# Kernel optimization log

Measured on AMD Instinct MI355X. Metric: run time of the kernel, lower is better.

The kernel has to match this reference:

```python
import jax, jax.numpy as jnp
import numpy as np

N_HEAD = 16
N_KV_HEAD = 4
HEAD_DIM = 128
D_MODEL = 2048
ROTARY_DIM = 128  # == head_dim
ROTARY_BASE = 10000
N_CTX = 2048
BATCH = 2
SEQ = 2048


def _rope_sincos(T, dtype):
    # Matches calculate_sin_cos_rotary with rotary_adjacent_pairs=False:
    # freq = base**(d/(rd/2)) for d in [0, rd/2), then tiled twice.
    pos = jnp.arange(T, dtype=jnp.float32)
    dim = jnp.arange(ROTARY_DIM // 2, dtype=jnp.float32)
    freq = jnp.asarray(ROTARY_BASE, jnp.float32) ** (dim / (ROTARY_DIM / 2))
    freq = jnp.concatenate([freq, freq])          # [rd]
    angles = pos[:, None] / freq[None, :]          # [T, rd]
    return jnp.sin(angles).astype(dtype), jnp.cos(angles).astype(dtype)


def _rotate_half(x):
    # rotate_every_two with adjacent_pairs=False: [-x2, x1] over halves
    n = x.shape[-1] // 2
    return jnp.concatenate([-x[..., n:], x[..., :n]], axis=-1)


def setup_inputs() -> dict:
    key = jax.random.key(0)
    kx, kq, kkv, kp = jax.random.split(key, 4)
    scale = 0.02
    return {
        "x": jax.random.normal(kx, (BATCH, SEQ, D_MODEL), jnp.float32),
        "Wq": jax.random.normal(kq, (D_MODEL, D_MODEL), jnp.float32) * scale,
        "Wkv": jax.random.normal(kkv, (2 * N_KV_HEAD * HEAD_DIM, D_MODEL), jnp.float32) * scale,
        "Wproj": jax.random.normal(kp, (D_MODEL, D_MODEL), jnp.float32) * scale,
    }


def reference(x, Wq, Wkv, Wproj):
    B, T, C = x.shape
    # QKV projections (torch Linear: y = x @ W.T)
    q = x @ Wq.T                                   # [B,T,C]
    kv = x @ Wkv.T                                 # [B,T,2*kv*hd]
    k, v = jnp.split(kv, 2, axis=2)
    q = q.reshape(B, T, N_HEAD, HEAD_DIM).transpose(0, 2, 1, 3)      # [B,H,T,d]
    k = k.reshape(B, T, N_KV_HEAD, HEAD_DIM).transpose(0, 2, 1, 3)   # [B,Hk,T,d]
    v = v.reshape(B, T, N_KV_HEAD, HEAD_DIM).transpose(0, 2, 1, 3)

    # RoPE: position_ids = arange(T) clamped at n_ctx-1 (identity for T<=n_ctx)
    sin, cos = _rope_sincos(T, q.dtype)            # [T, rd]
    sin = sin[None, None]                          # [1,1,T,rd]
    cos = cos[None, None]
    q = q * cos + _rotate_half(q) * sin
    k = k * cos + _rotate_half(k) * sin

    # GQA: expand kv heads (repeat_interleave along head dim)
    rep = N_HEAD // N_KV_HEAD
    k = jnp.repeat(k, rep, axis=1)                 # [B,H,T,d]
    v = jnp.repeat(v, rep, axis=1)

    # Causal SDPA
    scale = 1.0 / np.sqrt(HEAD_DIM)
    scores = jnp.einsum('bhqd,bhkd->bhqk', q, k) * scale
    causal = jnp.tril(jnp.ones((T, T), bool))
    scores = jnp.where(causal[None, None], scores, jnp.asarray(-jnp.inf, scores.dtype))
    attn = jax.nn.softmax(scores, axis=-1)
    y = jnp.einsum('bhqk,bhkd->bhqd', attn, v)     # [B,H,T,d]

    y = y.transpose(0, 2, 1, 3).reshape(B, T, C)
    return y @ Wproj.T
```

## Files before the change

kernel.cpp:

```cpp
#include <hip/hip_runtime.h>
#include <stdint.h>

#define T_SEQ 2048
#define D_MODEL 2048
#define N_KV 4
#define HD 128
#define QKV_W 3072

typedef unsigned short us;
typedef __attribute__((ext_vector_type(8))) short bf16x8;
typedef __attribute__((ext_vector_type(4))) float f32x4;
typedef __attribute__((ext_vector_type(8))) unsigned short u16x8;

__device__ __forceinline__ us f2bf(float f) {
  union { float f; unsigned int u; } v; v.f = f;
  unsigned int r = v.u + 0x7FFFu + ((v.u >> 16) & 1u);
  return (us)(r >> 16);
}
__device__ __forceinline__ float bf2f(us h) {
  union { unsigned int u; float f; } v; v.u = ((unsigned int)h) << 16;
  return v.f;
}

__device__ __forceinline__ void load_lds16(const void* g, void* l) {
  __builtin_amdgcn_global_load_lds(
      (const __attribute__((address_space(1))) void*)g,
      (__attribute__((address_space(3))) void*)l, 16, 0, 0);
}

__global__ void fill_diag(float* __restrict__ out, float val, int n) {
  int i = blockIdx.x * blockDim.x + threadIdx.x;
  if (i < n) out[i] = val;
}

__global__ void cast_f32_bf16(const float* __restrict__ src,
                              us* __restrict__ dst, int n8) {
  int i = blockIdx.x * blockDim.x + threadIdx.x;
  if (i >= n8) return;
  const float4* s = (const float4*)src + (size_t)i * 2;
  float4 a = s[0], b = s[1];
  u16x8 o;
  o[0] = f2bf(a.x); o[1] = f2bf(a.y); o[2] = f2bf(a.z); o[3] = f2bf(a.w);
  o[4] = f2bf(b.x); o[5] = f2bf(b.y); o[6] = f2bf(b.z); o[7] = f2bf(b.w);
  *((u16x8*)dst + i) = o;
}

template <typename OUT>
__global__ __launch_bounds__(256) void gemm_bt(
    const us* __restrict__ A, const us* __restrict__ B,
    OUT* __restrict__ C, int M, int N, int K) {
  __shared__ us As[2][128 * 32];
  __shared__ us Bs[2][128 * 32];

  const int tid  = threadIdx.x;
  const int lane = tid & 63;
  const int wave = tid >> 6;
  const int l15  = lane & 15;
  const int quad = lane >> 4;
  const int bm = blockIdx.x * 128;
  const int bn = blockIdx.y * 128;
  const int wm = (wave & 1) * 64;
  const int wn = (wave >> 1) * 64;

  f32x4 acc[4][4];
#pragma unroll
  for (int i = 0; i < 4; i++)
#pragma unroll
    for (int j = 0; j < 4; j++) acc[i][j] = (f32x4)0.f;

  const int srow = tid >> 2;
  const int scol = (tid & 3) * 8;
  const us* Ag = A + (size_t)(bm + srow) * K + scol;
  const us* Bg = B + (size_t)(bn + srow) * K + scol;
  const size_t rowskip = (size_t)64 * K;

#define STAGE(buf, koff)                                            \
  do {                                                              \
    load_lds16(Ag + (koff), &As[(buf)][tid * 8]);                   \
    load_lds16(Ag + (koff) + rowskip, &As[(buf)][tid * 8 + 2048]);  \
    load_lds16(Bg + (koff), &Bs[(buf)][tid * 8]);                   \
    load_lds16(Bg + (koff) + rowskip, &Bs[(buf)][tid * 8 + 2048]);  \
  } while (0)

  STAGE(0, 0);
  __syncthreads();

  int cur = 0;
  for (int k0 = 0; k0 < K; k0 += 32) {
    if (k0 + 32 < K) STAGE(cur ^ 1, k0 + 32);

    bf16x8 a[4], b[4];
#pragma unroll
    for (int mt = 0; mt < 4; mt++)
      a[mt] = *(const bf16x8*)&As[cur][(wm + mt * 16 + l15) * 32 + quad * 8];
#pragma unroll
    for (int nt = 0; nt < 4; nt++)
      b[nt] = *(const bf16x8*)&Bs[cur][(wn + nt * 16 + l15) * 32 + quad * 8];
#pragma unroll
    for (int mt = 0; mt < 4; mt++)
#pragma unroll
      for (int nt = 0; nt < 4; nt++)
        acc[mt][nt] = __builtin_amdgcn_mfma_f32_16x16x32_bf16(a[mt], b[nt], acc[mt][nt], 0, 0, 0);

    __syncthreads();
    cur ^= 1;
  }
#undef STAGE

#pragma unroll
  for (int mt = 0; mt < 4; mt++) {
    int row = bm + wm + mt * 16 + quad * 4;
#pragma unroll
    for (int nt = 0; nt < 4; nt++) {
      int col = bn + wn + nt * 16 + l15;
#pragma unroll
      for (int r = 0; r < 4; r++) {
        if constexpr (sizeof(OUT) == 4)
          C[(size_t)(row + r) * N + col] = acc[mt][nt][r];
        else
          C[(size_t)(row + r) * N + col] = f2bf(acc[mt][nt][r]);
      }
    }
  }
}

#define GBAR()                                  \
  do {                                          \
    asm volatile("" ::: "memory");              \
    __builtin_amdgcn_s_barrier();               \
    asm volatile("" ::: "memory");              \
  } while (0)
#define VMCNT6() asm volatile("s_waitcnt vmcnt(6)" ::: "memory")
#define VMCNT0() asm volatile("s_waitcnt vmcnt(0)" ::: "memory")

template <typename OUT>
__global__ __launch_bounds__(512) void gemm_bt8(
    const us* __restrict__ A, const us* __restrict__ B,
    OUT* __restrict__ C, int M, int N, int K) {
  __shared__ us As[2][16384];
  __shared__ us Bs[2][16384];

  const int tid  = threadIdx.x;
  const int lane = tid & 63;
  const int wave = tid >> 6;
  const int wm   = wave & 1;
  const int wn   = wave >> 1;
  const int l15  = lane & 15;
  const int quad = lane >> 4;
  const int bm = blockIdx.x * 256;
  const int bn = blockIdx.y * 256;
  const int wm8 = wm * 8;
  const int wn4 = wn * 4;

  const int ro = ((l15 << 5) | (quad << 3)) ^ ((l15 & 8) << 1);

  const int s    = lane ^ ((lane & 32) >> 4);
  const int srow = s >> 2;
  const int schk = (s & 3) * 8;

  const int R_Ae = (wave & 3) | ((wave & 4) << 1);
  const int R_Al = R_Ae + 4;
  const int R_Be = ((wave >> 1) << 2) | (wave & 1);
  const int R_Bl = R_Be + 2;

  const us* Ab = A + (size_t)bm * K;
  const us* Bb = B + (size_t)bn * K;

  f32x4 acc[8][4];
#pragma unroll
  for (int i = 0; i < 8; i++)
#pragma unroll
    for (int j = 0; j < 4; j++) acc[i][j] = (f32x4)0.f;

  bf16x8 af[4][2], bf[4][2];

#define STG(DST, PG, R, KT)                                                   \
  do {                                                                        \
    load_lds16((PG) + (size_t)((R) * 16 + srow) * K + (KT) * 64 + schk,       \
               &(DST)[(((R) * 2 + 0) << 9) + (lane << 3)]);                   \
    load_lds16((PG) + (size_t)((R) * 16 + srow) * K + (KT) * 64 + 32 + schk,  \
               &(DST)[(((R) * 2 + 1) << 9) + (lane << 3)]);                   \
  } while (0)

#define LDA4(BUF, MTB)                                                        \
  _Pragma("unroll") for (int t = 0; t < 4; t++)                               \
      _Pragma("unroll") for (int ks = 0; ks < 2; ks++)                        \
          af[t][ks] = *(const bf16x8*)&As[BUF][(((wm8 + (MTB) + t) * 2 + ks)  \
                                               << 9) + ro];

#define LDB2(BUF, NTB)                                                        \
  _Pragma("unroll") for (int t = 0; t < 2; t++)                               \
      _Pragma("unroll") for (int ks = 0; ks < 2; ks++)                        \
          bf[(NTB) + t][ks] = *(const bf16x8*)&Bs[BUF][                       \
              (((wn4 + (NTB) + t) * 2 + ks) << 9) + ro];

#define MQ(MH, NB)                                                            \
  __builtin_amdgcn_s_setprio(1);                                              \
  _Pragma("unroll") for (int t = 0; t < 4; t++)                               \
      _Pragma("unroll") for (int u = 0; u < 2; u++)                           \
          _Pragma("unroll") for (int ks = 0; ks < 2; ks++)                    \
              acc[(MH) * 4 + t][(NB) + u] =                                   \
                  __builtin_amdgcn_mfma_f32_16x16x32_bf16(                    \
                      af[t][ks], bf[(NB) + u][ks],                            \
                      acc[(MH) * 4 + t][(NB) + u], 0, 0, 0);                  \
  __builtin_amdgcn_s_setprio(0);

  STG(As[0], Ab, R_Ae, 0); STG(As[0], Ab, R_Al, 0);
  STG(Bs[0], Bb, R_Be, 0); STG(Bs[0], Bb, R_Bl, 0);
  STG(As[1], Ab, R_Ae, 1); STG(Bs[1], Bb, R_Be, 1); STG(Bs[1], Bb, R_Bl, 1);
  VMCNT6();
  GBAR();

  const int NI = K >> 7;
  for (int i = 0; i < NI - 1; i++) {
    const int t0 = 2 * i;
    LDA4(0, 0) LDB2(0, 0)
    STG(As[1], Ab, R_Al, t0 + 1);
    GBAR(); MQ(0, 0) GBAR();
    LDB2(0, 2)
    STG(As[0], Ab, R_Ae, t0 + 2);
    GBAR(); MQ(0, 2) GBAR();
    LDA4(0, 4)
    STG(Bs[0], Bb, R_Be, t0 + 2);
    GBAR(); MQ(1, 2) GBAR();
    STG(Bs[0], Bb, R_Bl, t0 + 2);
    GBAR(); MQ(1, 0) VMCNT6(); GBAR();
    LDA4(1, 0) LDB2(1, 0)
    STG(As[0], Ab, R_Al, t0 + 2);
    GBAR(); MQ(0, 0) GBAR();
    LDB2(1, 2)
    STG(As[1], Ab, R_Ae, t0 + 3);
    GBAR(); MQ(0, 2) GBAR();
    LDA4(1, 4)
    STG(Bs[1], Bb, R_Be, t0 + 3);
    GBAR(); MQ(1, 2) GBAR();
    STG(Bs[1], Bb, R_Bl, t0 + 3);
    GBAR(); MQ(1, 0) VMCNT6(); GBAR();
  }
  {
    const int t0 = 2 * NI - 2;
    LDA4(0, 0) LDB2(0, 0)
    STG(As[1], Ab, R_Al, t0 + 1);
    GBAR(); MQ(0, 0) GBAR();
    LDB2(0, 2)
    GBAR(); MQ(0, 2) GBAR();
    LDA4(0, 4)
    GBAR(); MQ(1, 2) GBAR();
    GBAR(); MQ(1, 0) VMCNT0(); GBAR();
    LDA4(1, 0) LDB2(1, 0)
    GBAR(); MQ(0, 0) GBAR();
    LDB2(1, 2)
    GBAR(); MQ(0, 2) GBAR();
    LDA4(1, 4)
    GBAR(); MQ(1, 2) GBAR();
    MQ(1, 0)
  }
#undef STG
#undef LDA4
#undef LDB2
#undef MQ

#pragma unroll
  for (int mt = 0; mt < 8; mt++) {
    int row = bm + wm * 128 + mt * 16 + quad * 4;
#pragma unroll
    for (int nt = 0; nt < 4; nt++) {
      int col = bn + wn * 64 + nt * 16 + l15;
#pragma unroll
      for (int r = 0; r < 4; r++) {
        if constexpr (sizeof(OUT) == 4)
          C[(size_t)(row + r) * N + col] = acc[mt][nt][r];
        else
          C[(size_t)(row + r) * N + col] = f2bf(acc[mt][nt][r]);
      }
    }
  }
}

__global__ void rope_kernel(us* __restrict__ qkv) {
  const int row = blockIdx.x;
  const int t = row & (T_SEQ - 1);
  const int tid = threadIdx.x;
  const float L2_10K_64 = 13.287712379549449f / 64.f;
  us* rp = qkv + (size_t)row * QKV_W;

#pragma unroll
  for (int it = 0; it < 4; it++) {
    int idx = it * 256 + tid;
    int h = idx >> 6, i = idx & 63;
    int base = h * HD;
    float ang = (float)t * exp2f(-(float)i * L2_10K_64);
    float s, c; sincosf(ang, &s, &c);
    float x1 = bf2f(rp[base + i]);
    float x2 = bf2f(rp[base + i + 64]);
    rp[base + i]      = f2bf(x1 * c - x2 * s);
    rp[base + i + 64] = f2bf(x2 * c + x1 * s);
  }
  {
    int h = tid >> 6, i = tid & 63;
    int base = 2048 + h * HD;
    float ang = (float)t * exp2f(-(float)i * L2_10K_64);
    float s, c; sincosf(ang, &s, &c);
    float x1 = bf2f(rp[base + i]);
    float x2 = bf2f(rp[base + i + 64]);
    rp[base + i]      = f2bf(x1 * c - x2 * s);
    rp[base + i + 64] = f2bf(x2 * c + x1 * s);
  }
}

__device__ __forceinline__ int vperm(int d) { return ((d >> 3) ^ d) & 7; }

__global__ __launch_bounds__(1024) void attn_kernel(
    const us* __restrict__ qkv, us* __restrict__ y) {
  __shared__ us Ks[64][136];
  __shared__ us Vt[128][64];
  __shared__ us Pl[16][2][16][40];

  const int tid  = threadIdx.x;
  const int lane = tid & 63;
  const int wave = tid >> 6;
  const int l15  = lane & 15;
  const int quad = lane >> 4;
  const int bh = blockIdx.y;
  const int b  = bh >> 4;
  const int h  = bh & 15;
  const int hk = h >> 2;
  const int p  = blockIdx.x;
  const int g  = wave >> 2;
  const int w4 = wave & 3;
  const int xA = 31 - p;
  const int x_mine = (g == 0) ? (31 - p)
                   : (g == 1) ? p
                   : (g == 2) ? (15 - p)
                              : (16 + p);
  const int m0 = x_mine * 64;

  const us* base = qkv + (size_t)b * T_SEQ * QKV_W;
  const int kcol = 2048 + hk * HD;
  const int vcol = kcol + 512;
  const int skey = tid >> 4;
  const int skk  = (tid & 15) * 8;
  const float scale = 0.12751744f;

  bf16x8 qf[4];
  {
    const us* Qrow = base + (size_t)(m0 + w4 * 16 + l15) * QKV_W + h * HD;
#pragma unroll
    for (int s = 0; s < 4; s++)
      qf[s] = *(const bf16x8*)&Qrow[s * 32 + quad * 8];
  }

  f32x4 O[8];
#pragma unroll
  for (int i = 0; i < 8; i++) O[i] = (f32x4)0.f;
  float mrun[4], lrun[4];
#pragma unroll
  for (int r = 0; r < 4; r++) { mrun[r] = -INFINITY; lrun[r] = 0.f; }

  uint4 kreg; u16x8 vreg;
  {
    const us* row = base + (size_t)skey * QKV_W;
    kreg = *(const uint4*)(row + kcol + skk);
    vreg = *(const u16x8*)(row + vcol + skk);
  }

  for (int j = 0; j <= xA; j++) {
    __syncthreads();
    *(uint4*)&Ks[skey][skk] = kreg;
#pragma unroll
    for (int i = 0; i < 8; i++) {
      int d = skk + i;
      Vt[d][skey ^ (vperm(d) << 3)] = vreg[i];
    }
    __syncthreads();

    if (j < xA) {
      const us* row = base + (size_t)((j + 1) * 64 + skey) * QKV_W;
      kreg = *(const uint4*)(row + kcol + skk);
      vreg = *(const u16x8*)(row + vcol + skk);
    }

    if (j <= x_mine) {
      f32x4 S[4];
      __builtin_amdgcn_s_setprio(1);
#pragma unroll
      for (int nt = 0; nt < 4; nt++) {
        f32x4 sa = (f32x4)0.f;
#pragma unroll
        for (int ks = 0; ks < 4; ks++) {
          bf16x8 kf = *(const bf16x8*)&Ks[nt * 16 + l15][ks * 32 + quad * 8];
          sa = __builtin_amdgcn_mfma_f32_16x16x32_bf16(qf[ks], kf, sa, 0, 0, 0);
        }
        S[nt] = sa;
      }
      __builtin_amdgcn_s_setprio(0);

      const int row0 = m0 + w4 * 16 + quad * 4;
      if (j == x_mine) {
        const int k0 = j * 64;
#pragma unroll
        for (int nt = 0; nt < 4; nt++) {
          int col = k0 + nt * 16 + l15;
#pragma unroll
          for (int r = 0; r < 4; r++) {
            float v = S[nt][r] * scale;
            if (col > row0 + r) v = -INFINITY;
            S[nt][r] = v;
          }
        }
      } else {
#pragma unroll
        for (int nt = 0; nt < 4; nt++)
#pragma unroll
          for (int r = 0; r < 4; r++) S[nt][r] *= scale;
      }

      float pr[4][4];
#pragma unroll
      for (int r = 0; r < 4; r++) {
        float mx = fmaxf(fmaxf(S[0][r], S[1][r]), fmaxf(S[2][r], S[3][r]));
#pragma unroll
        for (int off = 1; off < 16; off <<= 1)
          mx = fmaxf(mx, __shfl_xor(mx, off, 64));
        float mnew = fmaxf(mrun[r], mx);
        float alpha = exp2f(mrun[r] - mnew);
        mrun[r] = mnew;
        float sum = 0.f;
#pragma unroll
        for (int nt = 0; nt < 4; nt++) {
          float pv = exp2f(S[nt][r] - mnew);
          pr[nt][r] = pv;
          sum += pv;
        }
        lrun[r] = lrun[r] * alpha + sum;
#pragma unroll
        for (int ot = 0; ot < 8; ot++) O[ot][r] *= alpha;
      }

#pragma unroll
      for (int kh = 0; kh < 2; kh++) {
#pragma unroll
        for (int nt = 0; nt < 2; nt++)
#pragma unroll
          for (int r = 0; r < 4; r++)
            Pl[wave][kh][quad * 4 + r][nt * 16 + l15] = f2bf(pr[kh * 2 + nt][r]);
        bf16x8 pf = *(const bf16x8*)&Pl[wave][kh][l15][quad * 8];
        __builtin_amdgcn_s_setprio(1);
#pragma unroll
        for (int ot = 0; ot < 8; ot++) {
          int dcol = ot * 16 + l15;
          bf16x8 vf = *(const bf16x8*)&Vt[dcol][(kh * 32 + quad * 8) ^ (vperm(dcol) << 3)];
          O[ot] = __builtin_amdgcn_mfma_f32_16x16x32_bf16(pf, vf, O[ot], 0, 0, 0);
        }
        __builtin_amdgcn_s_setprio(0);
      }
    }
  }

  const int t_out = m0 + w4 * 16 + quad * 4;
#pragma unroll
  for (int r = 0; r < 4; r++) {
    float s = lrun[r];
#pragma unroll
    for (int off = 1; off < 16; off <<= 1)
      s += __shfl_xor(s, off, 64);
    float inv_l = 1.f / s;
    us* yrow = y + (size_t)(b * T_SEQ + t_out + r) * D_MODEL + h * HD;
#pragma unroll
    for (int ot = 0; ot < 8; ot++)
      yrow[ot * 16 + l15] = f2bf(O[ot][r] * inv_l);
  }
}

extern "C" void kernel_launch(void* const* d_in, const int* in_sizes, int n_in,
                              void* d_out, int out_size, void* d_ws, size_t ws_size,
                              hipStream_t stream) {
  const float* x     = (const float*)d_in[0];
  const float* Wq    = (const float*)d_in[1];
  const float* Wkv   = (const float*)d_in[2];
  const float* Wproj = (const float*)d_in[3];
  float* out = (float*)d_out;

  const size_t NX  = (size_t)4096 * 2048;
  const size_t NWQ = (size_t)2048 * 2048;
  const size_t NWK = (size_t)1024 * 2048;
  const size_t needed_ws = (NX + (NWQ + NWK) + NWQ + NX) * sizeof(us);

  int b0 = (n_in >= 1 && (size_t)in_sizes[0] == NX);
  int b1 = (n_in >= 2 && (size_t)in_sizes[1] == NWQ);
  int b2 = (n_in >= 3 && (size_t)in_sizes[2] == NWK);
  int b3 = (n_in >= 4 && (size_t)in_sizes[3] == NWQ);
  int ws_ok = (ws_size >= needed_ws);
  int out_ok = ((size_t)out_size == NX);
  if (!(n_in == 4 && b0 && b1 && b2 && b3 && ws_ok && out_ok)) {
    float code = 1.0e6f * (float)(n_in < 10 ? n_in : 9)
               + 1.0e5f * b0 + 1.0e4f * b1 + 1.0e3f * b2 + 1.0e2f * b3
               + 10.0f * ws_ok + 40.0f * out_ok;
    fill_diag<<<dim3((out_size + 255) / 256), dim3(256), 0, stream>>>(out, code, out_size);
    return;
  }

  us* xb     = (us*)d_ws;
  us* Wqkvb  = xb + NX;
  us* Wpb    = Wqkvb + NWQ + NWK;
  us* ybuf   = Wpb + NWQ;
  us* qkvbuf = (us*)d_out;

  dim3 blk(256);
  cast_f32_bf16<<<dim3((int)(NX  / 8 / 256)), blk, 0, stream>>>(x,     xb,          (int)(NX  / 8));
  cast_f32_bf16<<<dim3((int)(NWQ / 8 / 256)), blk, 0, stream>>>(Wq,    Wqkvb,       (int)(NWQ / 8));
  cast_f32_bf16<<<dim3((int)(NWK / 8 / 256)), blk, 0, stream>>>(Wkv,   Wqkvb + NWQ, (int)(NWK / 8));
  cast_f32_bf16<<<dim3((int)(NWQ / 8 / 256)), blk, 0, stream>>>(Wproj, Wpb,         (int)(NWQ / 8));

  gemm_bt8<us><<<dim3(16, 12), dim3(512), 0, stream>>>(xb, Wqkvb, qkvbuf, 4096, 3072, 2048);
  rope_kernel<<<dim3(4096), blk, 0, stream>>>(qkvbuf);
  attn_kernel<<<dim3(8, 32), dim3(1024), 0, stream>>>(qkvbuf, ybuf);
  gemm_bt<float><<<dim3(32, 16), blk, 0, stream>>>(ybuf, Wpb, out, 4096, 2048, 2048);
}
```

Before: 338.7 us.

## Use pipelined 256x128 GEMM for output projection and lazy softmax rescaling

Replaces the simple 128x128 double-buffered output-projection GEMM with a 512-thread 256x128 tile kernel. The new kernel interleaves LDS fragment loads, async global-to-LDS staging and MFMA bursts, using barriers, vmcnt waits and a swizzled LDS layout to hide load latency. In attention, the running-max update and rescale of O and l are skipped unless some row's max grows by more than 8 (log2 units) across the wave. This removes most per-tile exp2 and multiply work, at the cost of an extra wave vote and a looser bound on intermediate magnitudes.

```diff
diff --git a/kernel.cpp b/kernel.cpp
--- a/kernel.cpp
+++ b/kernel.cpp
@@ -45,85 +45,6 @@
   *((u16x8*)dst + i) = o;
 }
 
-template <typename OUT>
-__global__ __launch_bounds__(256) void gemm_bt(
-    const us* __restrict__ A, const us* __restrict__ B,
-    OUT* __restrict__ C, int M, int N, int K) {
-  __shared__ us As[2][128 * 32];
-  __shared__ us Bs[2][128 * 32];
-
-  const int tid  = threadIdx.x;
-  const int lane = tid & 63;
-  const int wave = tid >> 6;
-  const int l15  = lane & 15;
-  const int quad = lane >> 4;
-  const int bm = blockIdx.x * 128;
-  const int bn = blockIdx.y * 128;
-  const int wm = (wave & 1) * 64;
-  const int wn = (wave >> 1) * 64;
-
-  f32x4 acc[4][4];
-#pragma unroll
-  for (int i = 0; i < 4; i++)
-#pragma unroll
-    for (int j = 0; j < 4; j++) acc[i][j] = (f32x4)0.f;
-
-  const int srow = tid >> 2;
-  const int scol = (tid & 3) * 8;
-  const us* Ag = A + (size_t)(bm + srow) * K + scol;
-  const us* Bg = B + (size_t)(bn + srow) * K + scol;
-  const size_t rowskip = (size_t)64 * K;
-
-#define STAGE(buf, koff)                                            \
-  do {                                                              \
-    load_lds16(Ag + (koff), &As[(buf)][tid * 8]);                   \
-    load_lds16(Ag + (koff) + rowskip, &As[(buf)][tid * 8 + 2048]);  \
-    load_lds16(Bg + (koff), &Bs[(buf)][tid * 8]);                   \
-    load_lds16(Bg + (koff) + rowskip, &Bs[(buf)][tid * 8 + 2048]);  \
-  } while (0)
-
-  STAGE(0, 0);
-  __syncthreads();
-
-  int cur = 0;
-  for (int k0 = 0; k0 < K; k0 += 32) {
-    if (k0 + 32 < K) STAGE(cur ^ 1, k0 + 32);
-
-    bf16x8 a[4], b[4];
-#pragma unroll
-    for (int mt = 0; mt < 4; mt++)
-      a[mt] = *(const bf16x8*)&As[cur][(wm + mt * 16 + l15) * 32 + quad * 8];
-#pragma unroll
-    for (int nt = 0; nt < 4; nt++)
-      b[nt] = *(const bf16x8*)&Bs[cur][(wn + nt * 16 + l15) * 32 + quad * 8];
-#pragma unroll
-    for (int mt = 0; mt < 4; mt++)
-#pragma unroll
-      for (int nt = 0; nt < 4; nt++)
-        acc[mt][nt] = __builtin_amdgcn_mfma_f32_16x16x32_bf16(a[mt], b[nt], acc[mt][nt], 0, 0, 0);
-
-    __syncthreads();
-    cur ^= 1;
-  }
-#undef STAGE
-
-#pragma unroll
-  for (int mt = 0; mt < 4; mt++) {
-    int row = bm + wm + mt * 16 + quad * 4;
-#pragma unroll
-    for (int nt = 0; nt < 4; nt++) {
-      int col = bn + wn + nt * 16 + l15;
-#pragma unroll
-      for (int r = 0; r < 4; r++) {
-        if constexpr (sizeof(OUT) == 4)
-          C[(size_t)(row + r) * N + col] = acc[mt][nt][r];
-        else
-          C[(size_t)(row + r) * N + col] = f2bf(acc[mt][nt][r]);
-      }
-    }
-  }
-}
-
 #define GBAR()                                  \
   do {                                          \
     asm volatile("" ::: "memory");              \
@@ -131,6 +52,7 @@
     asm volatile("" ::: "memory");              \
   } while (0)
 #define VMCNT6() asm volatile("s_waitcnt vmcnt(6)" ::: "memory")
+#define VMCNT4() asm volatile("s_waitcnt vmcnt(4)" ::: "memory")
 #define VMCNT0() asm volatile("s_waitcnt vmcnt(0)" ::: "memory")
 
 template <typename OUT>
@@ -277,6 +199,142 @@
   }
 }
 
+template <typename OUT>
+__global__ __launch_bounds__(512) void gemm_bt8b(
+    const us* __restrict__ A, const us* __restrict__ B,
+    OUT* __restrict__ C, int M, int N, int K) {
+  __shared__ us As[2][16384];
+  __shared__ us Bs[2][8192];
+
+  const int tid  = threadIdx.x;
+  const int lane = tid & 63;
+  const int wave = tid >> 6;
+  const int wm   = wave & 1;
+  const int wn   = wave >> 1;
+  const int l15  = lane & 15;
+  const int quad = lane >> 4;
+  const int bm = blockIdx.x * 256;
+  const int bn = blockIdx.y * 128;
+  const int wm8 = wm * 8;
+  const int wn2 = wn * 2;
+
+  const int ro = ((l15 << 5) | (quad << 3)) ^ ((l15 & 8) << 1);
+
+  const int s    = lane ^ ((lane & 32) >> 4);
+  const int srow = s >> 2;
+  const int schk = (s & 3) * 8;
+
+  const int R_Ae = (wave & 3) | ((wave & 4) << 1);
+  const int R_Al = R_Ae + 4;
+  const int R_B  = wave;
+
+  const us* Ab = A + (size_t)bm * K;
+  const us* Bb = B + (size_t)bn * K;
+
+  f32x4 acc[8][2];
+#pragma unroll
+  for (int i = 0; i < 8; i++)
+#pragma unroll
+    for (int j = 0; j < 2; j++) acc[i][j] = (f32x4)0.f;
+
+  bf16x8 af[4][2], bf[2][2];
+
+#define STGB(DST, PG, R, KT)                                                  \
+  do {                                                                        \
+    load_lds16((PG) + (size_t)((R) * 16 + srow) * K + (KT) * 64 + schk,       \
+               &(DST)[(((R) * 2 + 0) << 9) + (lane << 3)]);                   \
+    load_lds16((PG) + (size_t)((R) * 16 + srow) * K + (KT) * 64 + 32 + schk,  \
+               &(DST)[(((R) * 2 + 1) << 9) + (lane << 3)]);                   \
+  } while (0)
+
+#define LDA4B(BUF, MTB)                                                       \
+  _Pragma("unroll") for (int t = 0; t < 4; t++)                               \
+      _Pragma("unroll") for (int ks = 0; ks < 2; ks++)                        \
+          af[t][ks] = *(const bf16x8*)&As[BUF][(((wm8 + (MTB) + t) * 2 + ks)  \
+                                               << 9) + ro];
+
+#define LDB1B(BUF, NT)                                                        \
+  _Pragma("unroll") for (int ks = 0; ks < 2; ks++)                            \
+      bf[NT][ks] = *(const bf16x8*)&Bs[BUF][(((wn2 + (NT)) * 2 + ks) << 9) +  \
+                                            ro];
+
+#define MQB(MH, NB)                                                           \
+  __builtin_amdgcn_s_setprio(1);                                              \
+  _Pragma("unroll") for (int t = 0; t < 4; t++)                               \
+      _Pragma("unroll") for (int ks = 0; ks < 2; ks++)                        \
+          acc[(MH) * 4 + t][NB] =                                             \
+              __builtin_amdgcn_mfma_f32_16x16x32_bf16(                        \
+                  af[t][ks], bf[NB][ks], acc[(MH) * 4 + t][NB], 0, 0, 0);     \
+  __builtin_amdgcn_s_setprio(0);
+
+  STGB(As[0], Ab, R_Ae, 0); STGB(As[0], Ab, R_Al, 0); STGB(Bs[0], Bb, R_B, 0);
+  STGB(As[1], Ab, R_Ae, 1); STGB(Bs[1], Bb, R_B, 1);
+  VMCNT4();
+  GBAR();
+
+  const int NI = K >> 7;
+  for (int i = 0; i < NI - 1; i++) {
+    const int t0 = 2 * i;
+    LDA4B(0, 0) LDB1B(0, 0)
+    STGB(As[1], Ab, R_Al, t0 + 1);
+    GBAR(); MQB(0, 0) GBAR();
+    LDB1B(0, 1)
+    STGB(As[0], Ab, R_Ae, t0 + 2);
+    GBAR(); MQB(0, 1) GBAR();
+    LDA4B(0, 4)
+    STGB(Bs[0], Bb, R_B, t0 + 2);
+    GBAR(); MQB(1, 1) GBAR();
+    GBAR(); MQB(1, 0) VMCNT4(); GBAR();
+    LDA4B(1, 0) LDB1B(1, 0)
+    STGB(As[0], Ab, R_Al, t0 + 2);
+    GBAR(); MQB(0, 0) GBAR();
+    LDB1B(1, 1)
+    STGB(As[1], Ab, R_Ae, t0 + 3);
+    GBAR(); MQB(0, 1) GBAR();
+    LDA4B(1, 4)
+    STGB(Bs[1], Bb, R_B, t0 + 3);
+    GBAR(); MQB(1, 1) GBAR();
+    GBAR(); MQB(1, 0) VMCNT4(); GBAR();
+  }
+  {
+    LDA4B(0, 0) LDB1B(0, 0)
+    STGB(As[1], Ab, R_Al, 2 * NI - 1);
+    GBAR(); MQB(0, 0) GBAR();
+    LDB1B(0, 1)
+    GBAR(); MQB(0, 1) GBAR();
+    LDA4B(0, 4)
+    GBAR(); MQB(1, 1) GBAR();
+    GBAR(); MQB(1, 0) VMCNT0(); GBAR();
+    LDA4B(1, 0) LDB1B(1, 0)
+    GBAR(); MQB(0, 0) GBAR();
+    LDB1B(1, 1)
+    GBAR(); MQB(0, 1) GBAR();
+    LDA4B(1, 4)
+    GBAR(); MQB(1, 1) GBAR();
+    MQB(1, 0)
+  }
+#undef STGB
+#undef LDA4B
+#undef LDB1B
+#undef MQB
+
+#pragma unroll
+  for (int mt = 0; mt < 8; mt++) {
+    int row = bm + wm * 128 + mt * 16 + quad * 4;
+#pragma unroll
+    for (int nt = 0; nt < 2; nt++) {
+      int col = bn + wn * 32 + nt * 16 + l15;
+#pragma unroll
+      for (int r = 0; r < 4; r++) {
+        if constexpr (sizeof(OUT) == 4)
+          C[(size_t)(row + r) * N + col] = acc[mt][nt][r];
+        else
+          C[(size_t)(row + r) * N + col] = f2bf(acc[mt][nt][r]);
+      }
+    }
+  }
+}
+
 __global__ void rope_kernel(us* __restrict__ qkv) {
   const int row = blockIdx.x;
   const int t = row & (T_SEQ - 1);
@@ -415,26 +473,39 @@
           for (int r = 0; r < 4; r++) S[nt][r] *= scale;
       }
 
+      float mx[4];
+#pragma unroll
+      for (int r = 0; r < 4; r++) {
+        float m = fmaxf(fmaxf(S[0][r], S[1][r]), fmaxf(S[2][r], S[3][r]));
+#pragma unroll
+        for (int off = 1; off < 16; off <<= 1)
+          m = fmaxf(m, __shfl_xor(m, off, 64));
+        mx[r] = m;
+      }
+      float growth = fmaxf(fmaxf(mx[0] - mrun[0], mx[1] - mrun[1]),
+                           fmaxf(mx[2] - mrun[2], mx[3] - mrun[3]));
+      if (!__all(growth <= 8.f)) {
+#pragma unroll
+        for (int r = 0; r < 4; r++) {
+          float mnew = fmaxf(mrun[r], mx[r]);
+          float alpha = exp2f(mrun[r] - mnew);
+          mrun[r] = mnew;
+          lrun[r] *= alpha;
+#pragma unroll
+          for (int ot = 0; ot < 8; ot++) O[ot][r] *= alpha;
+        }
+      }
       float pr[4][4];
 #pragma unroll
       for (int r = 0; r < 4; r++) {
-        float mx = fmaxf(fmaxf(S[0][r], S[1][r]), fmaxf(S[2][r], S[3][r]));
-#pragma unroll
-        for (int off = 1; off < 16; off <<= 1)
-          mx = fmaxf(mx, __shfl_xor(mx, off, 64));
-        float mnew = fmaxf(mrun[r], mx);
-        float alpha = exp2f(mrun[r] - mnew);
-        mrun[r] = mnew;
         float sum = 0.f;
 #pragma unroll
         for (int nt = 0; nt < 4; nt++) {
-          float pv = exp2f(S[nt][r] - mnew);
+          float pv = exp2f(S[nt][r] - mrun[r]);
           pr[nt][r] = pv;
           sum += pv;
         }
-        lrun[r] = lrun[r] * alpha + sum;
-#pragma unroll
-        for (int ot = 0; ot < 8; ot++) O[ot][r] *= alpha;
+        lrun[r] += sum;
       }
 
 #pragma unroll
@@ -515,5 +586,5 @@
   gemm_bt8<us><<<dim3(16, 12), dim3(512), 0, stream>>>(xb, Wqkvb, qkvbuf, 4096, 3072, 2048);
   rope_kernel<<<dim3(4096), blk, 0, stream>>>(qkvbuf);
   attn_kernel<<<dim3(8, 32), dim3(1024), 0, stream>>>(qkvbuf, ybuf);
-  gemm_bt<float><<<dim3(32, 16), blk, 0, stream>>>(ybuf, Wpb, out, 4096, 2048, 2048);
-}
+  gemm_bt8b<float><<<dim3(16, 16), dim3(512), 0, stream>>>(ybuf, Wpb, out, 4096, 2048, 2048);
+}
```

New measurement: 330.9 us. 1.02x faster.
